# Optimization experiments

Hardware: AMD Instinct MI355X
Metric: run time of the kernel (lower is better)

Reference implementation:

```python
import jax, jax.numpy as jnp
import numpy as np

N = 100000   # nodes
E = 1600000  # edges
DIMS = [1, 32, 64, 128, 64, 32, 1]  # channel path through the 6 GraphConv layers


def setup_inputs() -> dict:
    key = jax.random.key(0)
    ks = jax.random.split(key, 16)
    inp = {
        "x": jax.random.normal(ks[0], (N, 1), dtype=jnp.float32),
        "src": jax.random.randint(ks[1], (E,), 0, N, dtype=jnp.int64),
        "dst": jax.random.randint(ks[2], (E,), 0, N, dtype=jnp.int64),
    }
    for i in range(6):
        fi, fo = DIMS[i], DIMS[i + 1]
        inp[f"W{i}"] = jax.random.normal(ks[3 + i], (fi, fo), dtype=jnp.float32) / np.sqrt(fi).astype(np.float32)
        inp[f"b{i}"] = jnp.zeros((fo,), dtype=jnp.float32)
    return inp


def _norms(src, dst):
    # DGL GraphConv norm='both': src scaled by out_deg^{-1/2}, dst by in_deg^{-1/2}
    ones = jnp.ones((E,), dtype=jnp.float32)
    out_deg = jax.ops.segment_sum(ones, src, num_segments=N)
    in_deg = jax.ops.segment_sum(ones, dst, num_segments=N)
    ns = jnp.maximum(out_deg, 1.0) ** -0.5
    nd = jnp.maximum(in_deg, 1.0) ** -0.5
    return ns, nd


def _graph_conv(h, W, b, src, dst, ns, nd):
    fi, fo = W.shape
    if fi > fo:  # DGL applies W before aggregation when reducing dims
        h = h @ W
    h = h * ns[:, None]
    h = jax.ops.segment_sum(h[src], dst, num_segments=N)  # gather + scatter-add
    h = h * nd[:, None]
    if fi <= fo:
        h = h @ W
    return h + b


def reference(x, src, dst, W0, b0, W1, b1, W2, b2, W3, b3, W4, b4, W5, b5):
    ns, nd = _norms(src, dst)
    h = x
    Ws = [W0, W1, W2, W3, W4, W5]
    bs = [b0, b1, b2, b3, b4, b5]
    for W, b in zip(Ws, bs):
        h = _graph_conv(h, W, b, src, dst, ns, nd)
    # LeakyReLU(negative_slope=-1.0) == abs
    return jnp.where(h >= 0, h, -h)
```

## Files before the change

### kernel.cpp

```cpp
#include <hip/hip_runtime.h>
#include <math.h>


#define CAP 64
#define POISON 0xAAAAAAAAu
#define BATCH 8192
#define BSHIFT 9
#define BNODES 512

__global__ __launch_bounds__(256) void k_bin(
    const int* __restrict__ src, const int* __restrict__ dst,
    unsigned* __restrict__ bcur, unsigned* __restrict__ scur,
    unsigned* __restrict__ pairbuf, unsigned short* __restrict__ srcbuf,
    const float* __restrict__ W0, const float* __restrict__ b0,
    const float* __restrict__ W1, const float* __restrict__ b1,
    const float* __restrict__ W2, const float* __restrict__ b2,
    const float* __restrict__ W3, const float* __restrict__ b3,
    const float* __restrict__ W4, const float* __restrict__ b4,
    const float* __restrict__ W5, double* __restrict__ beta,
    int E, int NPB, int NBUCK, int BCAP) {
  __shared__ unsigned stage32[BATCH];
  __shared__ unsigned short stage16[BATCH];
  __shared__ unsigned char bkt[BATCH];
  __shared__ int cnt[256], run[256], gb[256], sc[256];
  __shared__ double dA[6 * 128], dB[6 * 128];
  int t = threadIdx.x;

  if (blockIdx.x == 0) {
    if (t < 32) { dA[0 * 128 + t] = (double)W0[t]; dA[1 * 128 + t] = (double)b0[t]; }
    __syncthreads();
    if (t < 64) {
      for (int r = 0; r < 2; ++r) {
        double s = 0; for (int k = 0; k < 32; ++k) s += dA[r * 128 + k] * (double)W1[k * 64 + t];
        dB[r * 128 + t] = s;
      }
      dB[2 * 128 + t] = (double)b1[t];
    }
    __syncthreads();
    if (t < 128) {
      for (int r = 0; r < 3; ++r) {
        double s = 0; for (int k = 0; k < 64; ++k) s += dB[r * 128 + k] * (double)W2[k * 128 + t];
        dA[r * 128 + t] = s;
      }
      dA[3 * 128 + t] = (double)b2[t];
    }
    __syncthreads();
    if (t < 64) {
      for (int r = 0; r < 4; ++r) {
        double s = 0; for (int k = 0; k < 128; ++k) s += dA[r * 128 + k] * (double)W3[k * 64 + t];
        dB[r * 128 + t] = s;
      }
      dB[4 * 128 + t] = (double)b3[t];
    }
    __syncthreads();
    if (t < 32) {
      for (int r = 0; r < 5; ++r) {
        double s = 0; for (int k = 0; k < 64; ++k) s += dB[r * 128 + k] * (double)W4[k * 32 + t];
        dA[r * 128 + t] = s;
      }
      dA[5 * 128 + t] = (double)b4[t];
    }
    __syncthreads();
    if (t < 6) {
      double s = 0; for (int k = 0; k < 32; ++k) s += dA[t * 128 + k] * (double)W5[k];
      beta[t] = s;
    }
    return;
  }

  bool isPair = ((int)blockIdx.x <= NPB);
  int pb = isPair ? ((int)blockIdx.x - 1) : ((int)blockIdx.x - 1 - NPB);
  int base = pb * BATCH;
  int len = E - base; if (len > BATCH) len = BATCH;

  cnt[t] = 0;
  __syncthreads();
  for (int k = 0; k < BATCH / 256; ++k) {
    int e = base + k * 256 + t;
    if (e < E) {
      int key = isPair ? dst[e] : src[e];
      atomicAdd(&cnt[key >> BSHIFT], 1);
    }
  }
  __syncthreads();
  int c = cnt[t];
  sc[t] = c;
  __syncthreads();
  for (int off = 1; off < 256; off <<= 1) {
    int v = sc[t];
    if (t >= off) v += sc[t - off];
    __syncthreads();
    sc[t] = v;
    __syncthreads();
  }
  if (t < NBUCK) {
    run[t] = sc[t] - c;
    unsigned* cur = isPair ? bcur : scur;
    gb[t] = (c > 0) ? (int)(atomicAdd(&cur[t], (unsigned)c) - POISON) : 0;
  }
  cnt[t] = 0;
  __syncthreads();
  for (int k = 0; k < BATCH / 256; ++k) {
    int e = base + k * 256 + t;
    if (e < E) {
      if (isPair) {
        int s = src[e], d = dst[e];
        int b = d >> BSHIFT;
        int r = atomicAdd(&cnt[b], 1);
        int idx = run[b] + r;
        stage32[idx] = ((unsigned)(d & (BNODES - 1)) << 23) | (unsigned)s;
        bkt[idx] = (unsigned char)b;
      } else {
        int s = src[e];
        int b = s >> BSHIFT;
        int r = atomicAdd(&cnt[b], 1);
        int idx = run[b] + r;
        stage16[idx] = (unsigned short)(s & (BNODES - 1));
        bkt[idx] = (unsigned char)b;
      }
    }
  }
  __syncthreads();
  for (int i = t; i < len; i += 256) {
    int b = bkt[i];
    int pos = gb[b] + (i - run[b]);
    if (pos < BCAP) {
      if (isPair) pairbuf[(size_t)b * BCAP + pos] = stage32[i];
      else        srcbuf[(size_t)b * BCAP + pos]  = stage16[i];
    }
  }
}

__global__ __launch_bounds__(256) void k_fill(
    const unsigned* __restrict__ pairbuf, const unsigned short* __restrict__ srcbuf,
    const unsigned* __restrict__ bcur, const unsigned* __restrict__ scur,
    int* __restrict__ csr, unsigned* __restrict__ cursor, unsigned* __restrict__ outdeg,
    int n, int NBUCK, int BCAP) {
  __shared__ int lcur[BNODES];
  int t = threadIdx.x;
  bool isPair = ((int)blockIdx.x < NBUCK);
  int b = isPair ? (int)blockIdx.x : ((int)blockIdx.x - NBUCK);
  int v0 = b << BSHIFT;
  for (int i = t; i < BNODES; i += 256) lcur[i] = 0;
  __syncthreads();
  int cntb = (int)((isPair ? bcur[b] : scur[b]) - POISON);
  if (cntb > BCAP) cntb = BCAP;
  if (isPair) {
    for (int i = t; i < cntb; i += 256) {
      unsigned v = pairbuf[(size_t)b * BCAP + i];
      int s  = (int)(v & 0x7FFFFFu);
      int ld = (int)(v >> 23);
      int slot = atomicAdd(&lcur[ld], 1);
      if (slot < CAP) csr[(size_t)(v0 + ld) * CAP + slot] = s;
    }
    __syncthreads();
    for (int i = t; i < BNODES; i += 256) {
      int node = v0 + i;
      if (node < n) cursor[node] = POISON + (unsigned)lcur[i];
    }
  } else {
    for (int i = t; i < cntb; i += 256) {
      int ld = (int)srcbuf[(size_t)b * BCAP + i];
      atomicAdd(&lcur[ld], 1);
    }
    __syncthreads();
    for (int i = t; i < BNODES; i += 256) {
      int node = v0 + i;
      if (node < n) outdeg[node] = POISON + (unsigned)lcur[i];
    }
  }
}

__global__ __launch_bounds__(256) void k_round1(
    const unsigned* __restrict__ outdeg, const unsigned* __restrict__ cursor,
    const float* __restrict__ x, const int* __restrict__ csr,
    const double* __restrict__ beta,
    double* __restrict__ carr, double* __restrict__ nsv, double* __restrict__ ndv,
    double* __restrict__ w1, int n) {
  int tid = blockIdx.x * blockDim.x + threadIdx.x;
  int v = tid >> 2, sub = tid & 3;
  if (v >= n) return;
  int raw = (int)(cursor[v] - POISON);
  int cnt = raw > CAP ? CAP : raw;
  const int* row = csr + (size_t)v * CAP;
  double s = 0.0;
  for (int i = sub; i < cnt; i += 4) {
    int u = row[i];
    int od = (int)(outdeg[u] - POISON); if (od < 1) od = 1;
    s += (double)x[u] / sqrt((double)od);
  }
  s += __shfl_xor(s, 1);
  s += __shfl_xor(s, 2);
  if (sub != 0) return;
  int odv = (int)(outdeg[v] - POISON); if (odv < 1) odv = 1;
  int idv = raw < 1 ? 1 : raw;
  double ns = 1.0 / sqrt((double)odv);
  double nd = 1.0 / sqrt((double)idv);
  carr[v] = ns * nd;
  nsv[v] = ns;
  ndv[v] = nd;
  w1[v] = (ns * nd) * (beta[0] * s) + beta[1] * ns;
}

__global__ __launch_bounds__(256) void k_round(
    const double* __restrict__ win, double* __restrict__ wout,
    const double* __restrict__ beta, int iB,
    const double* __restrict__ carr, const double* __restrict__ nsv,
    const double* __restrict__ ndv, const float* __restrict__ b5,
    float* __restrict__ out, const unsigned* __restrict__ cursor,
    const int* __restrict__ csr, int n) {
  int tid = blockIdx.x * blockDim.x + threadIdx.x;
  int v = tid >> 2, sub = tid & 3;
  if (v >= n) return;
  int cnt = (int)(cursor[v] - POISON); if (cnt > CAP) cnt = CAP;
  const int* row = csr + (size_t)v * CAP;
  double s = 0.0;
  for (int i = sub; i < cnt; i += 4) s += win[row[i]];
  s += __shfl_xor(s, 1);
  s += __shfl_xor(s, 2);
  if (sub != 0) return;
  if (iB >= 0) wout[v] = carr[v] * s + beta[iB] * nsv[v];
  else         out[v] = (float)fabs(ndv[v] * s + (double)b5[0]);
}

extern "C" void kernel_launch(void* const* d_in, const int* in_sizes, int n_in,
                              void* d_out, int out_size, void* d_ws, size_t ws_size,
                              hipStream_t stream) {
  const float* x  = (const float*)d_in[0];
  const int* src  = (const int*)d_in[1];
  const int* dst  = (const int*)d_in[2];
  const float* W0 = (const float*)d_in[3];  const float* b0 = (const float*)d_in[4];
  const float* W1 = (const float*)d_in[5];  const float* b1 = (const float*)d_in[6];
  const float* W2 = (const float*)d_in[7];  const float* b2 = (const float*)d_in[8];
  const float* W3 = (const float*)d_in[9];  const float* b3 = (const float*)d_in[10];
  const float* W4 = (const float*)d_in[11]; const float* b4 = (const float*)d_in[12];
  const float* W5 = (const float*)d_in[13]; const float* b5 = (const float*)d_in[14];
  const int n = in_sizes[0];
  const int E = in_sizes[1];
  float* out = (float*)d_out;

  const int NBUCK = (n + BNODES - 1) >> BSHIFT;
  const int NPB   = (E + BATCH - 1) / BATCH;
  const int BCAP  = E / NBUCK + E / (NBUCK * 4) + 256;

  char* wp = (char*)d_ws;
  size_t off = 0;
  auto alloc = [&](size_t bytes) -> char* {
    char* p = wp + off;
    off += (bytes + 255) & ~(size_t)255;
    return p;
  };
  unsigned* outdeg = (unsigned*)alloc((size_t)n * 4);
  unsigned* cursor = (unsigned*)alloc((size_t)n * 4);
  int* csr      = (int*)alloc((size_t)n * CAP * 4);
  double* carr  = (double*)alloc((size_t)n * 8);
  double* ndv   = (double*)alloc((size_t)n * 8);
  double* nsv   = (double*)alloc((size_t)n * 8);
  double* wA    = (double*)alloc((size_t)n * 8);
  double* wB    = (double*)alloc((size_t)n * 8);
  double* beta  = (double*)alloc(8 * 8);
  unsigned* bcur = (unsigned*)alloc((size_t)NBUCK * 4);
  unsigned* scur = (unsigned*)alloc((size_t)NBUCK * 4);
  unsigned* pairbuf = (unsigned*)alloc((size_t)NBUCK * BCAP * 4);
  unsigned short* srcbuf = (unsigned short*)alloc((size_t)NBUCK * BCAP * 2);

  const int tb = 256;
  k_bin<<<1 + 2 * NPB, tb, 0, stream>>>(
      src, dst, bcur, scur, pairbuf, srcbuf,
      W0, b0, W1, b1, W2, b2, W3, b3, W4, b4, W5, beta, E, NPB, NBUCK, BCAP);
  k_fill<<<2 * NBUCK, tb, 0, stream>>>(
      pairbuf, srcbuf, bcur, scur, csr, cursor, outdeg, n, NBUCK, BCAP);

  const int gn4 = (4 * n + tb - 1) / tb;
  k_round1<<<gn4, tb, 0, stream>>>(outdeg, cursor, x, csr, beta,
                                   carr, nsv, ndv, wA, n);
  k_round<<<gn4, tb, 0, stream>>>(wA, wB, beta, 2, carr, nsv, ndv, b5, out, cursor, csr, n);
  k_round<<<gn4, tb, 0, stream>>>(wB, wA, beta, 3, carr, nsv, ndv, b5, out, cursor, csr, n);
  k_round<<<gn4, tb, 0, stream>>>(wA, wB, beta, 4, carr, nsv, ndv, b5, out, cursor, csr, n);
  k_round<<<gn4, tb, 0, stream>>>(wB, wA, beta, 5, carr, nsv, ndv, b5, out, cursor, csr, n);
  k_round<<<gn4, tb, 0, stream>>>(wA, wB, beta, -1, carr, nsv, ndv, b5, out, cursor, csr, n);
}
```

Measured before the change: 216.1 us.

## Bin edges with per-bucket shared slots and fuse degree/norm computation into fill

The binning kernel drops the count/prefix-scan/reorder passes and gives each bucket fixed shared-memory slots. Edges that overflow a bucket's slots go straight to global memory through atomics, and each bucket then flushes with one wave-wide coalesced write. The fill kernel now handles both in-degree and out-degree buckets in one block and precomputes the norms plus a pre-scaled input y, so the special first-round kernel becomes a generic round and no longer does per-edge outdeg lookups or sqrt. This removes several block barriers, one pass over the edge batch, and scattered sqrt work. The cost is more global atomics when buckets overflow, and the shared union must fit MAXB buckets.

```diff
diff --git a/kernel.cpp b/kernel.cpp
--- a/kernel.cpp
+++ b/kernel.cpp
@@ -7,6 +7,8 @@
 #define BATCH 8192
 #define BSHIFT 9
 #define BNODES 512
+#define SLOTS 64
+#define MAXB 224
 
 __global__ __launch_bounds__(256) void k_bin(
     const int* __restrict__ src, const int* __restrict__ dst,
@@ -19,50 +21,50 @@
     const float* __restrict__ W4, const float* __restrict__ b4,
     const float* __restrict__ W5, double* __restrict__ beta,
     int E, int NPB, int NBUCK, int BCAP) {
-  __shared__ unsigned stage32[BATCH];
-  __shared__ unsigned short stage16[BATCH];
-  __shared__ unsigned char bkt[BATCH];
-  __shared__ int cnt[256], run[256], gb[256], sc[256];
-  __shared__ double dA[6 * 128], dB[6 * 128];
+  __shared__ union {
+    struct { unsigned stage[MAXB * SLOTS]; int cnt[MAXB]; int gb[MAXB]; } p;
+    struct { unsigned short stage[MAXB * SLOTS]; int cnt[MAXB]; int gb[MAXB]; } q;
+    struct { double A[6 * 128]; double B[6 * 128]; } w;
+  } sm;
   int t = threadIdx.x;
 
   if (blockIdx.x == 0) {
-    if (t < 32) { dA[0 * 128 + t] = (double)W0[t]; dA[1 * 128 + t] = (double)b0[t]; }
+    if (t < 32) { sm.w.A[0 * 128 + t] = (double)W0[t]; sm.w.A[1 * 128 + t] = (double)b0[t]; }
     __syncthreads();
     if (t < 64) {
       for (int r = 0; r < 2; ++r) {
-        double s = 0; for (int k = 0; k < 32; ++k) s += dA[r * 128 + k] * (double)W1[k * 64 + t];
-        dB[r * 128 + t] = s;
-      }
-      dB[2 * 128 + t] = (double)b1[t];
+        double s = 0; for (int k = 0; k < 32; ++k) s += sm.w.A[r * 128 + k] * (double)W1[k * 64 + t];
+        sm.w.B[r * 128 + t] = s;
+      }
+      sm.w.B[2 * 128 + t] = (double)b1[t];
     }
     __syncthreads();
     if (t < 128) {
       for (int r = 0; r < 3; ++r) {
-        double s = 0; for (int k = 0; k < 64; ++k) s += dB[r * 128 + k] * (double)W2[k * 128 + t];
-        dA[r * 128 + t] = s;
-      }
-      dA[3 * 128 + t] = (double)b2[t];
+        double s = 0; for (int k = 0; k < 64; ++k) s += sm.w.B[r * 128 + k] * (double)W2[k * 128 + t];
+        sm.w.A[r * 128 + t] = s;
+      }
+      sm.w.A[3 * 128 + t] = (double)b2[t];
     }
     __syncthreads();
     if (t < 64) {
       for (int r = 0; r < 4; ++r) {
-        double s = 0; for (int k = 0; k < 128; ++k) s += dA[r * 128 + k] * (double)W3[k * 64 + t];
-        dB[r * 128 + t] = s;
-      }
-      dB[4 * 128 + t] = (double)b3[t];
+        double s = 0; for (int k = 0; k < 128; ++k) s += sm.w.A[r * 128 + k] * (double)W3[k * 64 + t];
+        sm.w.B[r * 128 + t] = s;
+      }
+      sm.w.B[4 * 128 + t] = (double)b3[t];
     }
     __syncthreads();
     if (t < 32) {
       for (int r = 0; r < 5; ++r) {
-        double s = 0; for (int k = 0; k < 64; ++k) s += dB[r * 128 + k] * (double)W4[k * 32 + t];
-        dA[r * 128 + t] = s;
-      }
-      dA[5 * 128 + t] = (double)b4[t];
+        double s = 0; for (int k = 0; k < 64; ++k) s += sm.w.B[r * 128 + k] * (double)W4[k * 32 + t];
+        sm.w.A[r * 128 + t] = s;
+      }
+      sm.w.A[5 * 128 + t] = (double)b4[t];
     }
     __syncthreads();
     if (t < 6) {
-      double s = 0; for (int k = 0; k < 32; ++k) s += dA[t * 128 + k] * (double)W5[k];
+      double s = 0; for (int k = 0; k < 32; ++k) s += sm.w.A[t * 128 + k] * (double)W5[k];
       beta[t] = s;
     }
     return;
@@ -71,62 +73,72 @@
   bool isPair = ((int)blockIdx.x <= NPB);
   int pb = isPair ? ((int)blockIdx.x - 1) : ((int)blockIdx.x - 1 - NPB);
   int base = pb * BATCH;
-  int len = E - base; if (len > BATCH) len = BATCH;
-
-  cnt[t] = 0;
-  __syncthreads();
-  for (int k = 0; k < BATCH / 256; ++k) {
-    int e = base + k * 256 + t;
-    if (e < E) {
-      int key = isPair ? dst[e] : src[e];
-      atomicAdd(&cnt[key >> BSHIFT], 1);
-    }
-  }
-  __syncthreads();
-  int c = cnt[t];
-  sc[t] = c;
-  __syncthreads();
-  for (int off = 1; off < 256; off <<= 1) {
-    int v = sc[t];
-    if (t >= off) v += sc[t - off];
-    __syncthreads();
-    sc[t] = v;
-    __syncthreads();
-  }
-  if (t < NBUCK) {
-    run[t] = sc[t] - c;
-    unsigned* cur = isPair ? bcur : scur;
-    gb[t] = (c > 0) ? (int)(atomicAdd(&cur[t], (unsigned)c) - POISON) : 0;
-  }
-  cnt[t] = 0;
-  __syncthreads();
-  for (int k = 0; k < BATCH / 256; ++k) {
-    int e = base + k * 256 + t;
-    if (e < E) {
-      if (isPair) {
-        int s = src[e], d = dst[e];
+
+  if (isPair) {
+    for (int i = t; i < NBUCK; i += 256) sm.p.cnt[i] = 0;
+    __syncthreads();
+    for (int k = 0; k < BATCH / 256; ++k) {
+      int e = base + k * 256 + t;
+      if (e < E) {
+        int s_ = src[e], d = dst[e];
         int b = d >> BSHIFT;
-        int r = atomicAdd(&cnt[b], 1);
-        int idx = run[b] + r;
-        stage32[idx] = ((unsigned)(d & (BNODES - 1)) << 23) | (unsigned)s;
-        bkt[idx] = (unsigned char)b;
-      } else {
-        int s = src[e];
-        int b = s >> BSHIFT;
-        int r = atomicAdd(&cnt[b], 1);
-        int idx = run[b] + r;
-        stage16[idx] = (unsigned short)(s & (BNODES - 1));
-        bkt[idx] = (unsigned char)b;
-      }
-    }
-  }
-  __syncthreads();
-  for (int i = t; i < len; i += 256) {
-    int b = bkt[i];
-    int pos = gb[b] + (i - run[b]);
-    if (pos < BCAP) {
-      if (isPair) pairbuf[(size_t)b * BCAP + pos] = stage32[i];
-      else        srcbuf[(size_t)b * BCAP + pos]  = stage16[i];
+        unsigned pack = ((unsigned)(d & (BNODES - 1)) << 23) | (unsigned)s_;
+        int r = atomicAdd(&sm.p.cnt[b], 1);
+        if (r < SLOTS) sm.p.stage[b * SLOTS + r] = pack;
+        else {
+          unsigned p0 = atomicAdd(&bcur[b], 1u);
+          int pos = (int)(p0 - POISON);
+          if (pos < BCAP) pairbuf[(size_t)b * BCAP + pos] = pack;
+        }
+      }
+    }
+    __syncthreads();
+    for (int i = t; i < NBUCK; i += 256) {
+      int c = sm.p.cnt[i]; if (c > SLOTS) c = SLOTS;
+      sm.p.cnt[i] = c;
+      sm.p.gb[i] = (c > 0) ? (int)(atomicAdd(&bcur[i], (unsigned)c) - POISON) : 0;
+    }
+    __syncthreads();
+    int wv = t >> 6, ln = t & 63;
+    for (int b = wv; b < NBUCK; b += 4) {
+      int c = sm.p.cnt[b];
+      if (ln < c) {
+        int pos = sm.p.gb[b] + ln;
+        if (pos < BCAP) pairbuf[(size_t)b * BCAP + pos] = sm.p.stage[b * SLOTS + ln];
+      }
+    }
+  } else {
+    for (int i = t; i < NBUCK; i += 256) sm.q.cnt[i] = 0;
+    __syncthreads();
+    for (int k = 0; k < BATCH / 256; ++k) {
+      int e = base + k * 256 + t;
+      if (e < E) {
+        int s_ = src[e];
+        int b = s_ >> BSHIFT;
+        unsigned short pack = (unsigned short)(s_ & (BNODES - 1));
+        int r = atomicAdd(&sm.q.cnt[b], 1);
+        if (r < SLOTS) sm.q.stage[b * SLOTS + r] = pack;
+        else {
+          unsigned p0 = atomicAdd(&scur[b], 1u);
+          int pos = (int)(p0 - POISON);
+          if (pos < BCAP) srcbuf[(size_t)b * BCAP + pos] = pack;
+        }
+      }
+    }
+    __syncthreads();
+    for (int i = t; i < NBUCK; i += 256) {
+      int c = sm.q.cnt[i]; if (c > SLOTS) c = SLOTS;
+      sm.q.cnt[i] = c;
+      sm.q.gb[i] = (c > 0) ? (int)(atomicAdd(&scur[i], (unsigned)c) - POISON) : 0;
+    }
+    __syncthreads();
+    int wv = t >> 6, ln = t & 63;
+    for (int b = wv; b < NBUCK; b += 4) {
+      int c = sm.q.cnt[b];
+      if (ln < c) {
+        int pos = sm.q.gb[b] + ln;
+        if (pos < BCAP) srcbuf[(size_t)b * BCAP + pos] = sm.q.stage[b * SLOTS + ln];
+      }
     }
   }
 }
@@ -134,92 +146,63 @@
 __global__ __launch_bounds__(256) void k_fill(
     const unsigned* __restrict__ pairbuf, const unsigned short* __restrict__ srcbuf,
     const unsigned* __restrict__ bcur, const unsigned* __restrict__ scur,
-    int* __restrict__ csr, unsigned* __restrict__ cursor, unsigned* __restrict__ outdeg,
+    const float* __restrict__ x, const double* __restrict__ beta,
+    int* __restrict__ csr, int* __restrict__ cursor,
+    double2* __restrict__ cns, double* __restrict__ ndv, double* __restrict__ y,
     int n, int NBUCK, int BCAP) {
   __shared__ int lcur[BNODES];
+  __shared__ int ocur[BNODES];
   int t = threadIdx.x;
-  bool isPair = ((int)blockIdx.x < NBUCK);
-  int b = isPair ? (int)blockIdx.x : ((int)blockIdx.x - NBUCK);
+  int b = blockIdx.x;
   int v0 = b << BSHIFT;
-  for (int i = t; i < BNODES; i += 256) lcur[i] = 0;
+  for (int i = t; i < BNODES; i += 256) { lcur[i] = 0; ocur[i] = 0; }
   __syncthreads();
-  int cntb = (int)((isPair ? bcur[b] : scur[b]) - POISON);
-  if (cntb > BCAP) cntb = BCAP;
-  if (isPair) {
-    for (int i = t; i < cntb; i += 256) {
-      unsigned v = pairbuf[(size_t)b * BCAP + i];
-      int s  = (int)(v & 0x7FFFFFu);
-      int ld = (int)(v >> 23);
-      int slot = atomicAdd(&lcur[ld], 1);
-      if (slot < CAP) csr[(size_t)(v0 + ld) * CAP + slot] = s;
-    }
-    __syncthreads();
-    for (int i = t; i < BNODES; i += 256) {
-      int node = v0 + i;
-      if (node < n) cursor[node] = POISON + (unsigned)lcur[i];
-    }
-  } else {
-    for (int i = t; i < cntb; i += 256) {
-      int ld = (int)srcbuf[(size_t)b * BCAP + i];
-      atomicAdd(&lcur[ld], 1);
-    }
-    __syncthreads();
-    for (int i = t; i < BNODES; i += 256) {
-      int node = v0 + i;
-      if (node < n) outdeg[node] = POISON + (unsigned)lcur[i];
-    }
-  }
-}
-
-__global__ __launch_bounds__(256) void k_round1(
-    const unsigned* __restrict__ outdeg, const unsigned* __restrict__ cursor,
-    const float* __restrict__ x, const int* __restrict__ csr,
-    const double* __restrict__ beta,
-    double* __restrict__ carr, double* __restrict__ nsv, double* __restrict__ ndv,
-    double* __restrict__ w1, int n) {
+  int cb = (int)(bcur[b] - POISON); if (cb > BCAP) cb = BCAP;
+  for (int i = t; i < cb; i += 256) {
+    unsigned v = pairbuf[(size_t)b * BCAP + i];
+    int ld = (int)(v >> 23);
+    int s_ = (int)(v & 0x7FFFFFu);
+    int slot = atomicAdd(&lcur[ld], 1);
+    if (slot < CAP) csr[(size_t)(v0 + ld) * CAP + slot] = s_;
+  }
+  int cs = (int)(scur[b] - POISON); if (cs > BCAP) cs = BCAP;
+  for (int i = t; i < cs; i += 256) {
+    atomicAdd(&ocur[srcbuf[(size_t)b * BCAP + i]], 1);
+  }
+  __syncthreads();
+  double b0 = beta[0];
+  for (int i = t; i < BNODES; i += 256) {
+    int node = v0 + i;
+    if (node < n) {
+      int id = lcur[i], od = ocur[i];
+      int idc = id < 1 ? 1 : id, odc = od < 1 ? 1 : od;
+      double ns = 1.0 / sqrt((double)odc);
+      double nd = 1.0 / sqrt((double)idc);
+      cursor[node] = id > CAP ? CAP : id;
+      cns[node] = make_double2(ns * nd, ns);
+      ndv[node] = nd;
+      y[node] = b0 * ns * (double)x[node];
+    }
+  }
+}
+
+__global__ __launch_bounds__(256) void k_round(
+    const double* __restrict__ win, double* __restrict__ wout,
+    const double* __restrict__ beta, int iB,
+    const double2* __restrict__ cns, const double* __restrict__ ndv,
+    const float* __restrict__ b5, float* __restrict__ out,
+    const int* __restrict__ cursor, const int* __restrict__ csr, int n) {
   int tid = blockIdx.x * blockDim.x + threadIdx.x;
   int v = tid >> 2, sub = tid & 3;
   if (v >= n) return;
-  int raw = (int)(cursor[v] - POISON);
-  int cnt = raw > CAP ? CAP : raw;
-  const int* row = csr + (size_t)v * CAP;
-  double s = 0.0;
-  for (int i = sub; i < cnt; i += 4) {
-    int u = row[i];
-    int od = (int)(outdeg[u] - POISON); if (od < 1) od = 1;
-    s += (double)x[u] / sqrt((double)od);
-  }
-  s += __shfl_xor(s, 1);
-  s += __shfl_xor(s, 2);
-  if (sub != 0) return;
-  int odv = (int)(outdeg[v] - POISON); if (odv < 1) odv = 1;
-  int idv = raw < 1 ? 1 : raw;
-  double ns = 1.0 / sqrt((double)odv);
-  double nd = 1.0 / sqrt((double)idv);
-  carr[v] = ns * nd;
-  nsv[v] = ns;
-  ndv[v] = nd;
-  w1[v] = (ns * nd) * (beta[0] * s) + beta[1] * ns;
-}
-
-__global__ __launch_bounds__(256) void k_round(
-    const double* __restrict__ win, double* __restrict__ wout,
-    const double* __restrict__ beta, int iB,
-    const double* __restrict__ carr, const double* __restrict__ nsv,
-    const double* __restrict__ ndv, const float* __restrict__ b5,
-    float* __restrict__ out, const unsigned* __restrict__ cursor,
-    const int* __restrict__ csr, int n) {
-  int tid = blockIdx.x * blockDim.x + threadIdx.x;
-  int v = tid >> 2, sub = tid & 3;
-  if (v >= n) return;
-  int cnt = (int)(cursor[v] - POISON); if (cnt > CAP) cnt = CAP;
+  int cnt = cursor[v];
   const int* row = csr + (size_t)v * CAP;
   double s = 0.0;
   for (int i = sub; i < cnt; i += 4) s += win[row[i]];
   s += __shfl_xor(s, 1);
   s += __shfl_xor(s, 2);
   if (sub != 0) return;
-  if (iB >= 0) wout[v] = carr[v] * s + beta[iB] * nsv[v];
+  if (iB >= 0) { double2 c = cns[v]; wout[v] = c.x * s + beta[iB] * c.y; }
   else         out[v] = (float)fabs(ndv[v] * s + (double)b5[0]);
 }
 
@@ -250,17 +233,16 @@
     off += (bytes + 255) & ~(size_t)255;
     return p;
   };
-  unsigned* outdeg = (unsigned*)alloc((size_t)n * 4);
-  unsigned* cursor = (unsigned*)alloc((size_t)n * 4);
-  int* csr      = (int*)alloc((size_t)n * CAP * 4);
-  double* carr  = (double*)alloc((size_t)n * 8);
-  double* ndv   = (double*)alloc((size_t)n * 8);
-  double* nsv   = (double*)alloc((size_t)n * 8);
-  double* wA    = (double*)alloc((size_t)n * 8);
-  double* wB    = (double*)alloc((size_t)n * 8);
-  double* beta  = (double*)alloc(8 * 8);
-  unsigned* bcur = (unsigned*)alloc((size_t)NBUCK * 4);
-  unsigned* scur = (unsigned*)alloc((size_t)NBUCK * 4);
+  int* cursor      = (int*)alloc((size_t)n * 4);
+  int* csr         = (int*)alloc((size_t)n * CAP * 4);
+  double2* cns     = (double2*)alloc((size_t)n * 16);
+  double* ndv      = (double*)alloc((size_t)n * 8);
+  double* y        = (double*)alloc((size_t)n * 8);
+  double* wA       = (double*)alloc((size_t)n * 8);
+  double* wB       = (double*)alloc((size_t)n * 8);
+  double* beta     = (double*)alloc(8 * 8);
+  unsigned* bcur   = (unsigned*)alloc((size_t)NBUCK * 4);
+  unsigned* scur   = (unsigned*)alloc((size_t)NBUCK * 4);
   unsigned* pairbuf = (unsigned*)alloc((size_t)NBUCK * BCAP * 4);
   unsigned short* srcbuf = (unsigned short*)alloc((size_t)NBUCK * BCAP * 2);
 
@@ -268,15 +250,15 @@
   k_bin<<<1 + 2 * NPB, tb, 0, stream>>>(
       src, dst, bcur, scur, pairbuf, srcbuf,
       W0, b0, W1, b1, W2, b2, W3, b3, W4, b4, W5, beta, E, NPB, NBUCK, BCAP);
-  k_fill<<<2 * NBUCK, tb, 0, stream>>>(
-      pairbuf, srcbuf, bcur, scur, csr, cursor, outdeg, n, NBUCK, BCAP);
+  k_fill<<<NBUCK, tb, 0, stream>>>(
+      pairbuf, srcbuf, bcur, scur, x, beta,
+      csr, cursor, cns, ndv, y, n, NBUCK, BCAP);
 
   const int gn4 = (4 * n + tb - 1) / tb;
-  k_round1<<<gn4, tb, 0, stream>>>(outdeg, cursor, x, csr, beta,
-                                   carr, nsv, ndv, wA, n);
-  k_round<<<gn4, tb, 0, stream>>>(wA, wB, beta, 2, carr, nsv, ndv, b5, out, cursor, csr, n);
-  k_round<<<gn4, tb, 0, stream>>>(wB, wA, beta, 3, carr, nsv, ndv, b5, out, cursor, csr, n);
-  k_round<<<gn4, tb, 0, stream>>>(wA, wB, beta, 4, carr, nsv, ndv, b5, out, cursor, csr, n);
-  k_round<<<gn4, tb, 0, stream>>>(wB, wA, beta, 5, carr, nsv, ndv, b5, out, cursor, csr, n);
-  k_round<<<gn4, tb, 0, stream>>>(wA, wB, beta, -1, carr, nsv, ndv, b5, out, cursor, csr, n);
-}
+  k_round<<<gn4, tb, 0, stream>>>(y,  wA, beta, 1, cns, ndv, b5, out, cursor, csr, n);
+  k_round<<<gn4, tb, 0, stream>>>(wA, wB, beta, 2, cns, ndv, b5, out, cursor, csr, n);
+  k_round<<<gn4, tb, 0, stream>>>(wB, wA, beta, 3, cns, ndv, b5, out, cursor, csr, n);
+  k_round<<<gn4, tb, 0, stream>>>(wA, wB, beta, 4, cns, ndv, b5, out, cursor, csr, n);
+  k_round<<<gn4, tb, 0, stream>>>(wB, wA, beta, 5, cns, ndv, b5, out, cursor, csr, n);
+  k_round<<<gn4, tb, 0, stream>>>(wA, wB, beta, -1, cns, ndv, b5, out, cursor, csr, n);
+}
```

Result: faster. 209.6 us (-3.0%).
